# Optimization experiments

Measured on AMD Instinct MI355X. Metric: run time of the kernel, lower is better.

Reference implementation:

```python
import jax, jax.numpy as jnp
import numpy as np

N_FACES = 40000
N_EDGES = 60000
NNZ = 3 * N_FACES  # 3 boundary edges per triangular face
IN_CH = 512
MID_CH = 512
OUT_CH = 512


def setup_inputs() -> dict:
    key = jax.random.key(0)
    k1, k2, k3 = jax.random.split(key, 3)
    x = jax.random.normal(k1, (N_FACES, IN_CH), dtype=jnp.float32)
    # xavier-uniform-ish scale with gain 1.414 as in TopoModelX Conv.reset_parameters
    W1 = jax.random.normal(k2, (IN_CH, MID_CH), dtype=jnp.float32) * (1.414 / np.sqrt(IN_CH))
    W2 = jax.random.normal(k3, (MID_CH, OUT_CH), dtype=jnp.float32) * (1.414 / np.sqrt(MID_CH))
    # COO incidence B2 [n_edges, n_faces]: face f -> edges (3f)%E,(3f+1)%E,(3f+2)%E
    i = jnp.arange(NNZ)
    face_idx = (i // 3).astype(jnp.int32)
    edge_idx = (i % N_EDGES).astype(jnp.int32)
    vals = jnp.ones((NNZ,), dtype=jnp.float32)
    return {"x": x, "W1": W1, "W2": W2, "edge_idx": edge_idx, "face_idx": face_idx, "vals": vals}


def _spmm(rows, cols, vals, x, n_rows):
    # y[r, :] = sum_{nnz with row r} vals * x[col, :]
    return jax.ops.segment_sum(vals[:, None] * x[cols], rows, num_segments=n_rows)


def reference(x, W1, W2, edge_idx, face_idx, vals):
    # row sums of B2 and B2^T for aggr_norm
    deg_e = jax.ops.segment_sum(vals, edge_idx, num_segments=N_EDGES)  # [n_edges]
    deg_f = jax.ops.segment_sum(vals, face_idx, num_segments=N_FACES)  # [n_faces]
    # conv level1: faces -> edges
    h = _spmm(edge_idx, face_idx, vals, x @ W1, N_EDGES)  # [n_edges, mid]
    h = jax.nn.sigmoid(h / deg_e[:, None])
    # conv level2: edges -> faces (transpose incidence)
    y = _spmm(face_idx, edge_idx, vals, h @ W2, N_FACES)  # [n_faces, out]
    return jax.nn.sigmoid(y / deg_f[:, None])
```

## Files before the change

### kernel.cpp

```cpp
#include <hip/hip_runtime.h>
#include <cstdint>

#define N_FACES_C 40000
#define N_EDGES_C 60000
#define CH        512
#define ELL_PAD   8

typedef __bf16 bf16_t;
typedef __bf16 bf16x8 __attribute__((ext_vector_type(8)));
typedef float  f32x4  __attribute__((ext_vector_type(4)));
static_assert(sizeof(bf16x8) == 16, "bf16x8 must be 16B");

__device__ __forceinline__ float fast_sigmoid(float z) {
  float e = __builtin_amdgcn_exp2f(z * -1.44269504f);
  return __builtin_amdgcn_rcpf(1.0f + e);
}

__global__ void prep(const int* __restrict__ ei, const int* __restrict__ fi,
                     const void* __restrict__ vals, int nnz,
                     float* __restrict__ deg_e, float* __restrict__ deg_f,
                     int* __restrict__ cnt_e, int* __restrict__ cnt_f,
                     int* __restrict__ col_e, float* __restrict__ val_e,
                     int* __restrict__ col_f, float* __restrict__ val_f,
                     const void* __restrict__ W1, bf16_t* __restrict__ W1t,
                     const void* __restrict__ W2, bf16_t* __restrict__ W2t,
                     const float* __restrict__ X, bf16_t* __restrict__ Xb,
                     int nbFill) {
  __shared__ bf16_t tile[32][33];
  const bool isb = (((const unsigned int*)vals)[0] == 0x3F803F80u);
  const int b = blockIdx.x;
  if (b < nbFill) {
    int i = b * 256 + threadIdx.x;
    if (i < nnz) {
      float v = isb ? (float)((const bf16_t*)vals)[i] : ((const float*)vals)[i];
      int e = ei[i], f = fi[i];
      if ((unsigned)e < (unsigned)N_EDGES_C && (unsigned)f < (unsigned)N_FACES_C) {
        atomicAdd(&deg_e[e], v);
        atomicAdd(&deg_f[f], v);
        int pe = atomicAdd(&cnt_e[e], 1);
        if (pe < ELL_PAD) { col_e[e * ELL_PAD + pe] = f; val_e[e * ELL_PAD + pe] = v; }
        int pf = atomicAdd(&cnt_f[f], 1);
        if (pf < ELL_PAD) { col_f[f * ELL_PAD + pf] = e; val_f[f * ELL_PAD + pf] = v; }
      }
    }
  } else if (b < nbFill + 512) {
    int bb = b - nbFill;
    int bz = bb >> 8; bb &= 255;
    const void* W = bz ? W2 : W1;
    bf16_t*    Wt = bz ? W2t : W1t;
    int byy = (bb >> 4) * 32, bxx = (bb & 15) * 32;
    int tx = threadIdx.x & 31, ty = threadIdx.x >> 5;
#pragma unroll
    for (int r = 0; r < 32; r += 8) {
      size_t idx = (size_t)(byy + ty + r) * CH + bxx + tx;
      tile[ty + r][tx] = isb ? ((const bf16_t*)W)[idx] : (bf16_t)((const float*)W)[idx];
    }
    __syncthreads();
#pragma unroll
    for (int r = 0; r < 32; r += 8)
      Wt[(size_t)(bxx + ty + r) * CH + byy + tx] = tile[tx][ty + r];
  } else {
    if (isb) return;
    size_t i = (size_t)(b - nbFill - 512) * 256 + threadIdx.x;
    const float4* src = (const float4*)X + i * 2;
    float4 a = src[0];
    float4 c = src[1];
    bf16x8 v;
    v[0] = (bf16_t)a.x; v[1] = (bf16_t)a.y; v[2] = (bf16_t)a.z; v[3] = (bf16_t)a.w;
    v[4] = (bf16_t)c.x; v[5] = (bf16_t)c.y; v[6] = (bf16_t)c.z; v[7] = (bf16_t)c.w;
    *((bf16x8*)Xb + i) = v;
  }
}

template <int SIG>
__global__ void spmm_row(const int* __restrict__ cnt, const int* __restrict__ cols,
                         const float* __restrict__ vals, const bf16_t* __restrict__ X,
                         const float* __restrict__ deg, bf16_t* __restrict__ Y,
                         int nRows, int nCols) {
  int row = blockIdx.x * 4 + (threadIdx.x >> 6);
  if (row >= nRows) return;
  int lane = threadIdx.x & 63;
  int n = cnt[row];
  if (n > ELL_PAD) n = ELL_PAD;
  if (n < 0) n = 0;
  const int base = row * ELL_PAD;
  const int lofs = lane * 8;
  int cfirst = 0;
  if (n > 0) {
    cfirst = cols[base];
    if ((unsigned)cfirst >= (unsigned)nCols) cfirst = 0;
  }
  int   c4[4]; float v4[4];
#pragma unroll
  for (int p = 0; p < 4; ++p) {
    int c = cfirst; float v = 0.f;
    if (p < n) {
      c = cols[base + p];
      if ((unsigned)c >= (unsigned)nCols) c = 0;
      v = vals[base + p];
    }
    c4[p] = c; v4[p] = v;
  }
  bf16x8 xv[4];
#pragma unroll
  for (int p = 0; p < 4; ++p)
    xv[p] = *(const bf16x8*)(X + (size_t)c4[p] * CH + lofs);
  float acc[8];
#pragma unroll
  for (int t = 0; t < 8; ++t) acc[t] = 0.f;
#pragma unroll
  for (int p = 0; p < 4; ++p)
#pragma unroll
    for (int t = 0; t < 8; ++t) acc[t] += v4[p] * (float)xv[p][t];
  for (int p = 4; p < n; ++p) {
    int c = cols[base + p];
    if ((unsigned)c >= (unsigned)nCols) c = 0;
    float v = vals[base + p];
    bf16x8 q = *(const bf16x8*)(X + (size_t)c * CH + lofs);
#pragma unroll
    for (int t = 0; t < 8; ++t) acc[t] += v * (float)q[t];
  }
  float d = deg[row];
  float invd = (d != 0.f) ? (1.0f / d) : 0.f;
  bf16x8 o;
#pragma unroll
  for (int t = 0; t < 8; ++t) {
    float z = acc[t] * invd;
    o[t] = (bf16_t)(SIG ? fast_sigmoid(z) : z);
  }
  *(bf16x8*)(Y + (size_t)row * CH + lofs) = o;
}

__global__ __launch_bounds__(512)
void gemm_tile(const bf16_t* __restrict__ Aorig, const bf16_t* __restrict__ Acvt,
               const bf16_t* __restrict__ Bt, void* __restrict__ C, int M,
               const unsigned int* __restrict__ vals_bits, int do_sig, int final_out) {
  __shared__ __align__(16) bf16_t As[128 * 64];
  __shared__ __align__(16) bf16_t Bs[256 * 64];
  const int tid  = threadIdx.x;
  const int lane = tid & 63;
  const int wave = tid >> 6;
  const int r0 = blockIdx.y * 128;
  const int c0 = blockIdx.x * 256;
  const int wr = (wave >> 2) * 64;
  const int wc = (wave & 3) * 64;
  const int q   = lane >> 4;
  const int l16 = lane & 15;
  const int srow_base = wave * 8 + (lane >> 3);
  const int sslot = lane & 7;
  const bool isb = (vals_bits[0] == 0x3F803F80u);
  const bf16_t* A = isb ? Aorig : Acvt;

  f32x4 acc[4][4];
#pragma unroll
  for (int i = 0; i < 4; ++i)
#pragma unroll
    for (int j = 0; j < 4; ++j)
      acc[i][j] = (f32x4){0.f, 0.f, 0.f, 0.f};

  for (int kt = 0; kt < 8; ++kt) {
    const int kb = kt * 64;
#pragma unroll
    for (int i = 0; i < 2; ++i) {
      const int lr = i * 64 + srow_base;
      const int gofs = (sslot ^ (lr & 7)) * 8;
      int ra = r0 + lr; if (ra > M - 1) ra = M - 1;
      __builtin_amdgcn_global_load_lds((const __attribute__((address_space(1))) void*)(A + (size_t)ra * CH + kb + gofs),
                                       (__attribute__((address_space(3))) void*)(As + (i * 64 + wave * 8) * 64), 16, 0, 0);
    }
#pragma unroll
    for (int i = 0; i < 4; ++i) {
      const int lb = i * 64 + srow_base;
      const int gofs = (sslot ^ (lb & 7)) * 8;
      __builtin_amdgcn_global_load_lds((const __attribute__((address_space(1))) void*)(Bt + (size_t)(c0 + lb) * CH + kb + gofs),
                                       (__attribute__((address_space(3))) void*)(Bs + (i * 64 + wave * 8) * 64), 16, 0, 0);
    }
    __syncthreads();

#pragma unroll
    for (int kk = 0; kk < 2; ++kk) {
      const int slot = (kk * 4 + q) ^ (l16 & 7);
      const int ro = slot * 8;
      bf16x8 af[4], bfv[4];
#pragma unroll
      for (int i = 0; i < 4; ++i)
        af[i] = *(const bf16x8*)(As + (wr + i * 16 + l16) * 64 + ro);
#pragma unroll
      for (int j = 0; j < 4; ++j)
        bfv[j] = *(const bf16x8*)(Bs + (wc + j * 16 + l16) * 64 + ro);
#pragma unroll
      for (int i = 0; i < 4; ++i)
#pragma unroll
        for (int j = 0; j < 4; ++j)
          acc[i][j] = __builtin_amdgcn_mfma_f32_16x16x32_bf16(af[i], bfv[j], acc[i][j], 0, 0, 0);
    }
    __syncthreads();
  }

  const bool f32out = final_out && !isb;
#pragma unroll
  for (int i = 0; i < 4; ++i) {
#pragma unroll
    for (int r = 0; r < 4; ++r) {
      int row = r0 + wr + i * 16 + q * 4 + r;
      if (row < M) {
#pragma unroll
        for (int j = 0; j < 4; ++j) {
          int col = c0 + wc + j * 16 + l16;
          float s = acc[i][j][r];
          if (do_sig) s = fast_sigmoid(s);
          if (f32out) ((float*)C)[(size_t)row * CH + col] = s;
          else        ((bf16_t*)C)[(size_t)row * CH + col] = (bf16_t)s;
        }
      }
    }
  }
}

extern "C" void kernel_launch(void* const* d_in, const int* in_sizes, int n_in,
                              void* d_out, int out_size, void* d_ws, size_t ws_size,
                              hipStream_t stream) {
  const void* x    = d_in[0];
  const void* W1   = d_in[1];
  const void* W2   = d_in[2];
  const int*  ei   = (const int*)d_in[3];
  const int*  fi   = (const int*)d_in[4];
  const void* vals = d_in[5];
  const int nnz = in_sizes[3];
  const unsigned int* vbits = (const unsigned int*)vals;

  char* ws = (char*)d_ws;
  size_t off = 0;
  auto alloc = [&](size_t bytes) -> void* {
    void* p = ws + off;
    off = (off + bytes + 511) & ~((size_t)511);
    return p;
  };
  bf16_t* t    = (bf16_t*)alloc((size_t)N_FACES_C * CH * 2);
  bf16_t* h    = (bf16_t*)alloc((size_t)N_EDGES_C * CH * 2);
  bf16_t* g    = (bf16_t*)alloc((size_t)N_FACES_C * CH * 2);
  bf16_t* xb   = g;
  bf16_t* w1t  = (bf16_t*)alloc((size_t)CH * CH * 2);
  bf16_t* w2t  = (bf16_t*)alloc((size_t)CH * CH * 2);
  float* deg_e = (float*)alloc((size_t)N_EDGES_C * 4);
  float* deg_f = (float*)alloc((size_t)N_FACES_C * 4);
  int*   cnt_e = (int*)alloc((size_t)N_EDGES_C * 4);
  int*   cnt_f = (int*)alloc((size_t)N_FACES_C * 4);
  size_t zero_bytes = (size_t)((char*)cnt_f + (size_t)N_FACES_C * 4 - (char*)deg_e);
  int*   col_e = (int*)alloc((size_t)N_EDGES_C * ELL_PAD * 4);
  float* val_e = (float*)alloc((size_t)N_EDGES_C * ELL_PAD * 4);
  int*   col_f = (int*)alloc((size_t)N_FACES_C * ELL_PAD * 4);
  float* val_f = (float*)alloc((size_t)N_FACES_C * ELL_PAD * 4);

  hipMemsetAsync(deg_e, 0, zero_bytes, stream);

  int nbFill = (nnz + 255) / 256;
  int nbCvt  = N_FACES_C * CH / 8 / 256;
  prep<<<nbFill + 512 + nbCvt, 256, 0, stream>>>(ei, fi, vals, nnz,
                                                 deg_e, deg_f, cnt_e, cnt_f,
                                                 col_e, val_e, col_f, val_f,
                                                 W1, w1t, W2, w2t,
                                                 (const float*)x, xb, nbFill);

  dim3 gemmGrid(CH / 256, (N_FACES_C + 127) / 128);

  gemm_tile<<<gemmGrid, 512, 0, stream>>>((const bf16_t*)x, xb, w1t, t, N_FACES_C,
                                          vbits, 0, 0);
  spmm_row<1><<<(N_EDGES_C + 3) / 4, 256, 0, stream>>>(cnt_e, col_e, val_e, t, deg_e, h,
                                                       N_EDGES_C, N_FACES_C);
  spmm_row<0><<<(N_FACES_C + 3) / 4, 256, 0, stream>>>(cnt_f, col_f, val_f, h, deg_f, g,
                                                       N_FACES_C, N_EDGES_C);
  gemm_tile<<<gemmGrid, 512, 0, stream>>>(g, g, w2t, d_out, N_FACES_C,
                                          vbits, 1, 1);
}
```

Before: 287.9 us.

## Fuse second SpMM gather into final GEMM and retile first GEMM to 128x128

The edges-to-faces SpMM is folded into the last GEMM's A-tile load. Each block gathers up to ELL_PAD rows of h, scales them by 1/deg, writes the result into LDS and multiplies against the full 512-column W2. This removes the intermediate g buffer, so one global write and one read of a 40000x512 bf16 matrix are skipped. The first GEMM also moves to 128x128 tiles with 256 threads. The fused kernel uses 64-row blocks with a 64KB B tile that is reloaded per block, and its gather is not overlapped with the MFMA work, which could limit occupancy and hide latency poorly.

Measured after the change: 296.1 us. 1.03x slower.

```diff
diff --git a/kernel.cpp b/kernel.cpp
--- a/kernel.cpp
+++ b/kernel.cpp
@@ -72,8 +72,7 @@
   }
 }
 
-template <int SIG>
-__global__ void spmm_row(const int* __restrict__ cnt, const int* __restrict__ cols,
+__global__ void spmm_sig(const int* __restrict__ cnt, const int* __restrict__ cols,
                          const float* __restrict__ vals, const bf16_t* __restrict__ X,
                          const float* __restrict__ deg, bf16_t* __restrict__ Y,
                          int nRows, int nCols) {
@@ -116,34 +115,32 @@
     int c = cols[base + p];
     if ((unsigned)c >= (unsigned)nCols) c = 0;
     float v = vals[base + p];
-    bf16x8 q = *(const bf16x8*)(X + (size_t)c * CH + lofs);
-#pragma unroll
-    for (int t = 0; t < 8; ++t) acc[t] += v * (float)q[t];
+    bf16x8 qv = *(const bf16x8*)(X + (size_t)c * CH + lofs);
+#pragma unroll
+    for (int t = 0; t < 8; ++t) acc[t] += v * (float)qv[t];
   }
   float d = deg[row];
   float invd = (d != 0.f) ? (1.0f / d) : 0.f;
   bf16x8 o;
 #pragma unroll
-  for (int t = 0; t < 8; ++t) {
-    float z = acc[t] * invd;
-    o[t] = (bf16_t)(SIG ? fast_sigmoid(z) : z);
-  }
+  for (int t = 0; t < 8; ++t)
+    o[t] = (bf16_t)fast_sigmoid(acc[t] * invd);
   *(bf16x8*)(Y + (size_t)row * CH + lofs) = o;
 }
 
-__global__ __launch_bounds__(512)
+__global__ __launch_bounds__(256)
 void gemm_tile(const bf16_t* __restrict__ Aorig, const bf16_t* __restrict__ Acvt,
                const bf16_t* __restrict__ Bt, void* __restrict__ C, int M,
                const unsigned int* __restrict__ vals_bits, int do_sig, int final_out) {
   __shared__ __align__(16) bf16_t As[128 * 64];
-  __shared__ __align__(16) bf16_t Bs[256 * 64];
+  __shared__ __align__(16) bf16_t Bs[128 * 64];
   const int tid  = threadIdx.x;
   const int lane = tid & 63;
   const int wave = tid >> 6;
   const int r0 = blockIdx.y * 128;
-  const int c0 = blockIdx.x * 256;
-  const int wr = (wave >> 2) * 64;
-  const int wc = (wave & 3) * 64;
+  const int c0 = blockIdx.x * 128;
+  const int wr = (wave >> 1) * 64;
+  const int wc = (wave & 1) * 64;
   const int q   = lane >> 4;
   const int l16 = lane & 15;
   const int srow_base = wave * 8 + (lane >> 3);
@@ -161,19 +158,16 @@
   for (int kt = 0; kt < 8; ++kt) {
     const int kb = kt * 64;
 #pragma unroll
-    for (int i = 0; i < 2; ++i) {
-      const int lr = i * 64 + srow_base;
+    for (int i = 0; i < 4; ++i) {
+      const int lr = i * 32 + srow_base;
       const int gofs = (sslot ^ (lr & 7)) * 8;
       int ra = r0 + lr; if (ra > M - 1) ra = M - 1;
-      __builtin_amdgcn_global_load_lds((const __attribute__((address_space(1))) void*)(A + (size_t)ra * CH + kb + gofs),
-                                       (__attribute__((address_space(3))) void*)(As + (i * 64 + wave * 8) * 64), 16, 0, 0);
-    }
-#pragma unroll
-    for (int i = 0; i < 4; ++i) {
-      const int lb = i * 64 + srow_base;
-      const int gofs = (sslot ^ (lb & 7)) * 8;
-      __builtin_amdgcn_global_load_lds((const __attribute__((address_space(1))) void*)(Bt + (size_t)(c0 + lb) * CH + kb + gofs),
-                                       (__attribute__((address_space(3))) void*)(Bs + (i * 64 + wave * 8) * 64), 16, 0, 0);
+      const bf16_t* ga = A  + (size_t)ra * CH + kb + gofs;
+      const bf16_t* gb = Bt + (size_t)(c0 + lr) * CH + kb + gofs;
+      __builtin_amdgcn_global_load_lds((const __attribute__((address_space(1))) void*)ga,
+                                       (__attribute__((address_space(3))) void*)(As + (i * 32 + wave * 8) * 64), 16, 0, 0);
+      __builtin_amdgcn_global_load_lds((const __attribute__((address_space(1))) void*)gb,
+                                       (__attribute__((address_space(3))) void*)(Bs + (i * 32 + wave * 8) * 64), 16, 0, 0);
     }
     __syncthreads();
 
@@ -209,6 +203,132 @@
           int col = c0 + wc + j * 16 + l16;
           float s = acc[i][j][r];
           if (do_sig) s = fast_sigmoid(s);
+          if (f32out) ((float*)C)[(size_t)row * CH + col] = s;
+          else        ((bf16_t*)C)[(size_t)row * CH + col] = (bf16_t)s;
+        }
+      }
+    }
+  }
+}
+
+__global__ __launch_bounds__(512, 4)
+void gemm_gather_sig(const int* __restrict__ cnt, const int* __restrict__ cols,
+                     const float* __restrict__ vals, const bf16_t* __restrict__ H,
+                     const float* __restrict__ deg, const bf16_t* __restrict__ Bt,
+                     void* __restrict__ C, int M, int nColsH,
+                     const unsigned int* __restrict__ vals_bits) {
+  __shared__ __align__(16) bf16_t As[64 * 64];
+  __shared__ __align__(16) bf16_t Bs[512 * 64];
+  const int tid  = threadIdx.x;
+  const int lane = tid & 63;
+  const int wave = tid >> 6;
+  const int r0 = blockIdx.x * 64;
+  const int q   = lane >> 4;
+  const int l16 = lane & 15;
+  const int srow_base = wave * 8 + (lane >> 3);
+  const int sslot = lane & 7;
+  const int lr = tid >> 3;
+  const int aslot = tid & 7;
+  const int agofs = (aslot ^ (lr & 7)) * 8;
+  int arow = r0 + lr; if (arow > M - 1) arow = M - 1;
+
+  int n = cnt[arow];
+  if (n > ELL_PAD) n = ELL_PAD;
+  if (n < 0) n = 0;
+  const int base = arow * ELL_PAD;
+  int cfirst = 0;
+  if (n > 0) {
+    cfirst = cols[base];
+    if ((unsigned)cfirst >= (unsigned)nColsH) cfirst = 0;
+  }
+  const bf16_t* hp[4];
+  float v4[4];
+#pragma unroll
+  for (int p = 0; p < 4; ++p) {
+    int c = cfirst; float v = 0.f;
+    if (p < n) {
+      c = cols[base + p];
+      if ((unsigned)c >= (unsigned)nColsH) c = 0;
+      v = vals[base + p];
+    }
+    hp[p] = H + (size_t)c * CH + agofs;
+    v4[p] = v;
+  }
+  float d = deg[arow];
+  const float invd = (d != 0.f) ? (1.0f / d) : 0.f;
+
+  const int bgofs = (sslot ^ (srow_base & 7)) * 8;
+
+  f32x4 acc[4][4];
+#pragma unroll
+  for (int i = 0; i < 4; ++i)
+#pragma unroll
+    for (int j = 0; j < 4; ++j)
+      acc[i][j] = (f32x4){0.f, 0.f, 0.f, 0.f};
+
+  for (int kt = 0; kt < 8; ++kt) {
+    const int kb = kt * 64;
+#pragma unroll
+    for (int i = 0; i < 8; ++i) {
+      const int brow = i * 64 + srow_base;
+      __builtin_amdgcn_global_load_lds((const __attribute__((address_space(1))) void*)(Bt + (size_t)brow * CH + kb + bgofs),
+                                       (__attribute__((address_space(3))) void*)(Bs + (i * 64 + wave * 8) * 64), 16, 0, 0);
+    }
+    float a8[8];
+#pragma unroll
+    for (int t = 0; t < 8; ++t) a8[t] = 0.f;
+#pragma unroll
+    for (int p = 0; p < 4; ++p) {
+      bf16x8 hv = *(const bf16x8*)(hp[p] + kb);
+      float v = v4[p];
+#pragma unroll
+      for (int t = 0; t < 8; ++t) a8[t] += v * (float)hv[t];
+    }
+    for (int p = 4; p < n; ++p) {
+      int c = cols[base + p];
+      if ((unsigned)c >= (unsigned)nColsH) c = 0;
+      float v = vals[base + p];
+      bf16x8 hv = *(const bf16x8*)(H + (size_t)c * CH + kb + agofs);
+#pragma unroll
+      for (int t = 0; t < 8; ++t) a8[t] += v * (float)hv[t];
+    }
+    bf16x8 av;
+#pragma unroll
+    for (int t = 0; t < 8; ++t) av[t] = (bf16_t)(a8[t] * invd);
+    *(bf16x8*)(As + lr * 64 + aslot * 8) = av;
+    __syncthreads();
+
+#pragma unroll
+    for (int kk = 0; kk < 2; ++kk) {
+      const int slot = (kk * 4 + q) ^ (l16 & 7);
+      const int ro = slot * 8;
+      bf16x8 af[4], bfv[4];
+#pragma unroll
+      for (int i = 0; i < 4; ++i)
+        af[i] = *(const bf16x8*)(As + (i * 16 + l16) * 64 + ro);
+#pragma unroll
+      for (int j = 0; j < 4; ++j)
+        bfv[j] = *(const bf16x8*)(Bs + (wave * 64 + j * 16 + l16) * 64 + ro);
+#pragma unroll
+      for (int i = 0; i < 4; ++i)
+#pragma unroll
+        for (int j = 0; j < 4; ++j)
+          acc[i][j] = __builtin_amdgcn_mfma_f32_16x16x32_bf16(af[i], bfv[j], acc[i][j], 0, 0, 0);
+    }
+    __syncthreads();
+  }
+
+  const bool f32out = (vals_bits[0] != 0x3F803F80u);
+#pragma unroll
+  for (int i = 0; i < 4; ++i) {
+#pragma unroll
+    for (int r = 0; r < 4; ++r) {
+      int row = r0 + i * 16 + q * 4 + r;
+      if (row < M) {
+#pragma unroll
+        for (int j = 0; j < 4; ++j) {
+          int col = wave * 64 + j * 16 + l16;
+          float s = fast_sigmoid(acc[i][j][r]);
           if (f32out) ((float*)C)[(size_t)row * CH + col] = s;
           else        ((bf16_t*)C)[(size_t)row * CH + col] = (bf16_t)s;
         }
@@ -238,8 +358,7 @@
   };
   bf16_t* t    = (bf16_t*)alloc((size_t)N_FACES_C * CH * 2);
   bf16_t* h    = (bf16_t*)alloc((size_t)N_EDGES_C * CH * 2);
-  bf16_t* g    = (bf16_t*)alloc((size_t)N_FACES_C * CH * 2);
-  bf16_t* xb   = g;
+  bf16_t* xb   = (bf16_t*)alloc((size_t)N_FACES_C * CH * 2);
   bf16_t* w1t  = (bf16_t*)alloc((size_t)CH * CH * 2);
   bf16_t* w2t  = (bf16_t*)alloc((size_t)CH * CH * 2);
   float* deg_e = (float*)alloc((size_t)N_EDGES_C * 4);
@@ -262,14 +381,10 @@
                                                  W1, w1t, W2, w2t,
                                                  (const float*)x, xb, nbFill);
 
-  dim3 gemmGrid(CH / 256, (N_FACES_C + 127) / 128);
-
-  gemm_tile<<<gemmGrid, 512, 0, stream>>>((const bf16_t*)x, xb, w1t, t, N_FACES_C,
-                                          vbits, 0, 0);
-  spmm_row<1><<<(N_EDGES_C + 3) / 4, 256, 0, stream>>>(cnt_e, col_e, val_e, t, deg_e, h,
-                                                       N_EDGES_C, N_FACES_C);
-  spmm_row<0><<<(N_FACES_C + 3) / 4, 256, 0, stream>>>(cnt_f, col_f, val_f, h, deg_f, g,
-                                                       N_FACES_C, N_EDGES_C);
-  gemm_tile<<<gemmGrid, 512, 0, stream>>>(g, g, w2t, d_out, N_FACES_C,
-                                          vbits, 1, 1);
-}
+  gemm_tile<<<dim3(CH / 128, (N_FACES_C + 127) / 128), 256, 0, stream>>>(
+      (const bf16_t*)x, xb, w1t, t, N_FACES_C, vbits, 0, 0);
+  spmm_sig<<<(N_EDGES_C + 3) / 4, 256, 0, stream>>>(cnt_e, col_e, val_e, t, deg_e, h,
+                                                    N_EDGES_C, N_FACES_C);
+  gemm_gather_sig<<<(N_FACES_C + 63) / 64, 512, 0, stream>>>(
+      cnt_f, col_f, val_f, h, deg_f, w2t, d_out, N_FACES_C, N_EDGES_C, vbits);
+}
```

## Fuse both SpMM hops into one kernel and shrink GEMM tile to 128x128

Applied to the files above, without the earlier changes.

Replaces the two sparse aggregation kernels with one two-hop kernel. Each face gathers its edges, recomputes every edge's sum over faces plus its sigmoid on the fly, then accumulates. This drops the 60000x512 intermediate edge buffer and its write and re-read, but each edge's value is recomputed by every face that touches it (about twice here) and the gathers from T are more scattered. Separately, the GEMM tile goes from 128x256 with 512 threads to 128x128 with 256 threads, which doubles the block count and cuts LDS per block, and xb now gets its own buffer.

After: 312.9 us. +8.7%, slower.

```diff
diff --git a/kernel.cpp b/kernel.cpp
--- a/kernel.cpp
+++ b/kernel.cpp
@@ -72,78 +72,139 @@
   }
 }
 
-template <int SIG>
-__global__ void spmm_row(const int* __restrict__ cnt, const int* __restrict__ cols,
-                         const float* __restrict__ vals, const bf16_t* __restrict__ X,
-                         const float* __restrict__ deg, bf16_t* __restrict__ Y,
-                         int nRows, int nCols) {
+__global__ void spmm_2hop(const int* __restrict__ cnt_f, const int* __restrict__ col_f,
+                          const float* __restrict__ val_f,
+                          const int* __restrict__ cnt_e, const int* __restrict__ col_e,
+                          const float* __restrict__ val_e,
+                          const float* __restrict__ deg_e, const float* __restrict__ deg_f,
+                          const bf16_t* __restrict__ T, bf16_t* __restrict__ G) {
   int row = blockIdx.x * 4 + (threadIdx.x >> 6);
-  if (row >= nRows) return;
-  int lane = threadIdx.x & 63;
-  int n = cnt[row];
-  if (n > ELL_PAD) n = ELL_PAD;
-  if (n < 0) n = 0;
-  const int base = row * ELL_PAD;
+  if (row >= N_FACES_C) return;
+  const int lane = threadIdx.x & 63;
   const int lofs = lane * 8;
-  int cfirst = 0;
-  if (n > 0) {
-    cfirst = cols[base];
-    if ((unsigned)cfirst >= (unsigned)nCols) cfirst = 0;
-  }
-  int   c4[4]; float v4[4];
+
+  int nf = cnt_f[row];
+  if (nf > ELL_PAD) nf = ELL_PAD;
+  if (nf < 0) nf = 0;
+  const int basef = row * ELL_PAD;
+  int efirst = 0;
+  if (nf > 0) {
+    efirst = col_f[basef];
+    if ((unsigned)efirst >= (unsigned)N_EDGES_C) efirst = 0;
+  }
+
+  int   ee[4];  float vf[4];  int ne_[4];  float invde[4];
+  int   cc[4][2]; float cv[4][2];
 #pragma unroll
   for (int p = 0; p < 4; ++p) {
-    int c = cfirst; float v = 0.f;
-    if (p < n) {
-      c = cols[base + p];
-      if ((unsigned)c >= (unsigned)nCols) c = 0;
-      v = vals[base + p];
-    }
-    c4[p] = c; v4[p] = v;
-  }
-  bf16x8 xv[4];
+    int e = efirst; float v = 0.f;
+    if (p < nf) {
+      e = col_f[basef + p];
+      if ((unsigned)e >= (unsigned)N_EDGES_C) e = 0;
+      v = val_f[basef + p];
+    }
+    ee[p] = e; vf[p] = v;
+    int ne = cnt_e[e];
+    if (ne > ELL_PAD) ne = ELL_PAD;
+    if (ne < 0) ne = 0;
+    ne_[p] = ne;
+    float de = deg_e[e];
+    invde[p] = (de != 0.f) ? (1.0f / de) : 0.f;
+    const int basee = e * ELL_PAD;
+    int cfirst = 0;
+    if (ne > 0) {
+      cfirst = col_e[basee];
+      if ((unsigned)cfirst >= (unsigned)N_FACES_C) cfirst = 0;
+    }
+#pragma unroll
+    for (int q = 0; q < 2; ++q) {
+      int c = cfirst; float vv = 0.f;
+      if (q < ne) {
+        c = col_e[basee + q];
+        if ((unsigned)c >= (unsigned)N_FACES_C) c = 0;
+        vv = val_e[basee + q];
+      }
+      cc[p][q] = c; cv[p][q] = vv;
+    }
+  }
+
+  bf16x8 tv[4][2];
 #pragma unroll
   for (int p = 0; p < 4; ++p)
-    xv[p] = *(const bf16x8*)(X + (size_t)c4[p] * CH + lofs);
-  float acc[8];
-#pragma unroll
-  for (int t = 0; t < 8; ++t) acc[t] = 0.f;
-#pragma unroll
-  for (int p = 0; p < 4; ++p)
-#pragma unroll
-    for (int t = 0; t < 8; ++t) acc[t] += v4[p] * (float)xv[p][t];
-  for (int p = 4; p < n; ++p) {
-    int c = cols[base + p];
-    if ((unsigned)c >= (unsigned)nCols) c = 0;
-    float v = vals[base + p];
-    bf16x8 q = *(const bf16x8*)(X + (size_t)c * CH + lofs);
-#pragma unroll
-    for (int t = 0; t < 8; ++t) acc[t] += v * (float)q[t];
-  }
-  float d = deg[row];
-  float invd = (d != 0.f) ? (1.0f / d) : 0.f;
+#pragma unroll
+    for (int q = 0; q < 2; ++q)
+      tv[p][q] = *(const bf16x8*)(T + (size_t)cc[p][q] * CH + lofs);
+
+  float accg[8];
+#pragma unroll
+  for (int t = 0; t < 8; ++t) accg[t] = 0.f;
+
+#pragma unroll
+  for (int p = 0; p < 4; ++p) {
+    float se[8];
+#pragma unroll
+    for (int t = 0; t < 8; ++t)
+      se[t] = cv[p][0] * (float)tv[p][0][t] + cv[p][1] * (float)tv[p][1][t];
+    for (int q = 2; q < ne_[p]; ++q) {
+      const int basee = ee[p] * ELL_PAD;
+      int c = col_e[basee + q];
+      if ((unsigned)c >= (unsigned)N_FACES_C) c = 0;
+      float vv = val_e[basee + q];
+      bf16x8 xv = *(const bf16x8*)(T + (size_t)c * CH + lofs);
+#pragma unroll
+      for (int t = 0; t < 8; ++t) se[t] += vv * (float)xv[t];
+    }
+    const float vp = vf[p], id = invde[p];
+#pragma unroll
+    for (int t = 0; t < 8; ++t)
+      accg[t] += vp * fast_sigmoid(se[t] * id);
+  }
+  for (int p = 4; p < nf; ++p) {
+    int e = col_f[basef + p];
+    if ((unsigned)e >= (unsigned)N_EDGES_C) e = 0;
+    float v = val_f[basef + p];
+    int ne = cnt_e[e];
+    if (ne > ELL_PAD) ne = ELL_PAD;
+    if (ne < 0) ne = 0;
+    float de = deg_e[e];
+    float id = (de != 0.f) ? (1.0f / de) : 0.f;
+    const int basee = e * ELL_PAD;
+    float se[8];
+#pragma unroll
+    for (int t = 0; t < 8; ++t) se[t] = 0.f;
+    for (int q = 0; q < ne; ++q) {
+      int c = col_e[basee + q];
+      if ((unsigned)c >= (unsigned)N_FACES_C) c = 0;
+      float vv = val_e[basee + q];
+      bf16x8 xv = *(const bf16x8*)(T + (size_t)c * CH + lofs);
+#pragma unroll
+      for (int t = 0; t < 8; ++t) se[t] += vv * (float)xv[t];
+    }
+#pragma unroll
+    for (int t = 0; t < 8; ++t) accg[t] += v * fast_sigmoid(se[t] * id);
+  }
+
+  float df = deg_f[row];
+  const float invdf = (df != 0.f) ? (1.0f / df) : 0.f;
   bf16x8 o;
 #pragma unroll
-  for (int t = 0; t < 8; ++t) {
-    float z = acc[t] * invd;
-    o[t] = (bf16_t)(SIG ? fast_sigmoid(z) : z);
-  }
-  *(bf16x8*)(Y + (size_t)row * CH + lofs) = o;
-}
-
-__global__ __launch_bounds__(512)
+  for (int t = 0; t < 8; ++t) o[t] = (bf16_t)(accg[t] * invdf);
+  *(bf16x8*)(G + (size_t)row * CH + lofs) = o;
+}
+
+__global__ __launch_bounds__(256)
 void gemm_tile(const bf16_t* __restrict__ Aorig, const bf16_t* __restrict__ Acvt,
                const bf16_t* __restrict__ Bt, void* __restrict__ C, int M,
                const unsigned int* __restrict__ vals_bits, int do_sig, int final_out) {
   __shared__ __align__(16) bf16_t As[128 * 64];
-  __shared__ __align__(16) bf16_t Bs[256 * 64];
+  __shared__ __align__(16) bf16_t Bs[128 * 64];
   const int tid  = threadIdx.x;
   const int lane = tid & 63;
   const int wave = tid >> 6;
   const int r0 = blockIdx.y * 128;
-  const int c0 = blockIdx.x * 256;
-  const int wr = (wave >> 2) * 64;
-  const int wc = (wave & 3) * 64;
+  const int c0 = blockIdx.x * 128;
+  const int wr = (wave >> 1) * 64;
+  const int wc = (wave & 1) * 64;
   const int q   = lane >> 4;
   const int l16 = lane & 15;
   const int srow_base = wave * 8 + (lane >> 3);
@@ -161,19 +222,16 @@
   for (int kt = 0; kt < 8; ++kt) {
     const int kb = kt * 64;
 #pragma unroll
-    for (int i = 0; i < 2; ++i) {
-      const int lr = i * 64 + srow_base;
+    for (int i = 0; i < 4; ++i) {
+      const int lr = i * 32 + srow_base;
       const int gofs = (sslot ^ (lr & 7)) * 8;
       int ra = r0 + lr; if (ra > M - 1) ra = M - 1;
-      __builtin_amdgcn_global_load_lds((const __attribute__((address_space(1))) void*)(A + (size_t)ra * CH + kb + gofs),
-                                       (__attribute__((address_space(3))) void*)(As + (i * 64 + wave * 8) * 64), 16, 0, 0);
-    }
-#pragma unroll
-    for (int i = 0; i < 4; ++i) {
-      const int lb = i * 64 + srow_base;
-      const int gofs = (sslot ^ (lb & 7)) * 8;
-      __builtin_amdgcn_global_load_lds((const __attribute__((address_space(1))) void*)(Bt + (size_t)(c0 + lb) * CH + kb + gofs),
-                                       (__attribute__((address_space(3))) void*)(Bs + (i * 64 + wave * 8) * 64), 16, 0, 0);
+      const bf16_t* ga = A  + (size_t)ra * CH + kb + gofs;
+      const bf16_t* gb = Bt + (size_t)(c0 + lr) * CH + kb + gofs;
+      __builtin_amdgcn_global_load_lds((const __attribute__((address_space(1))) void*)ga,
+                                       (__attribute__((address_space(3))) void*)(As + (i * 32 + wave * 8) * 64), 16, 0, 0);
+      __builtin_amdgcn_global_load_lds((const __attribute__((address_space(1))) void*)gb,
+                                       (__attribute__((address_space(3))) void*)(Bs + (i * 32 + wave * 8) * 64), 16, 0, 0);
     }
     __syncthreads();
 
@@ -237,9 +295,8 @@
     return p;
   };
   bf16_t* t    = (bf16_t*)alloc((size_t)N_FACES_C * CH * 2);
-  bf16_t* h    = (bf16_t*)alloc((size_t)N_EDGES_C * CH * 2);
   bf16_t* g    = (bf16_t*)alloc((size_t)N_FACES_C * CH * 2);
-  bf16_t* xb   = g;
+  bf16_t* xb   = (bf16_t*)alloc((size_t)N_FACES_C * CH * 2);
   bf16_t* w1t  = (bf16_t*)alloc((size_t)CH * CH * 2);
   bf16_t* w2t  = (bf16_t*)alloc((size_t)CH * CH * 2);
   float* deg_e = (float*)alloc((size_t)N_EDGES_C * 4);
@@ -262,14 +319,11 @@
                                                  W1, w1t, W2, w2t,
                                                  (const float*)x, xb, nbFill);
 
-  dim3 gemmGrid(CH / 256, (N_FACES_C + 127) / 128);
-
-  gemm_tile<<<gemmGrid, 512, 0, stream>>>((const bf16_t*)x, xb, w1t, t, N_FACES_C,
-                                          vbits, 0, 0);
-  spmm_row<1><<<(N_EDGES_C + 3) / 4, 256, 0, stream>>>(cnt_e, col_e, val_e, t, deg_e, h,
-                                                       N_EDGES_C, N_FACES_C);
-  spmm_row<0><<<(N_FACES_C + 3) / 4, 256, 0, stream>>>(cnt_f, col_f, val_f, h, deg_f, g,
-                                                       N_FACES_C, N_EDGES_C);
-  gemm_tile<<<gemmGrid, 512, 0, stream>>>(g, g, w2t, d_out, N_FACES_C,
-                                          vbits, 1, 1);
-}
+  gemm_tile<<<dim3(CH / 128, (N_FACES_C + 127) / 128), 256, 0, stream>>>(
+      (const bf16_t*)x, xb, w1t, t, N_FACES_C, vbits, 0, 0);
+  spmm_2hop<<<(N_FACES_C + 3) / 4, 256, 0, stream>>>(cnt_f, col_f, val_f,
+                                                     cnt_e, col_e, val_e,
+                                                     deg_e, deg_f, t, g);
+  gemm_tile<<<dim3(CH / 128, (N_FACES_C + 127) / 128), 256, 0, stream>>>(
+      g, g, w2t, d_out, N_FACES_C, vbits, 1, 1);
+}
```
